# Kernel optimization log

Measured on AMD Instinct MI355X. Metric: run time of the kernel, lower is better.

Reference implementation:

```python
import jax, jax.numpy as jnp
import numpy as np

N = 200000
E = 3200000
DIN = 275
H = 64
A = 14


def setup_inputs() -> dict:
    key = jax.random.key(0)
    ks = jax.random.split(key, 16)
    s = 0.05
    return {
        "inputs": jax.random.normal(ks[0], (N, DIN), jnp.float32),
        "hidden_state": jax.random.normal(ks[1], (N, H), jnp.float32),
        "edge_index": jax.random.randint(ks[2], (2, E), 0, N, jnp.int64),
        # Encoder
        "enc_w": jax.random.normal(ks[3], (H, DIN), jnp.float32) * s,
        "enc_b": jnp.zeros((H,), jnp.float32),
        # GRUCell (torch layout: [3H, in], gate order r,z,n)
        "w_ih": jax.random.normal(ks[4], (3 * H, H), jnp.float32) * s,
        "w_hh": jax.random.normal(ks[5], (3 * H, H), jnp.float32) * s,
        "b_ih": jnp.zeros((3 * H,), jnp.float32),
        "b_hh": jnp.zeros((3 * H,), jnp.float32),
        # GCNConv layers (PyG: weight [out,in], bias added after aggregation)
        "g1_w": jax.random.normal(ks[6], (H, H), jnp.float32) * s,
        "g1_b": jnp.zeros((H,), jnp.float32),
        "g2_w": jax.random.normal(ks[7], (H, H), jnp.float32) * s,
        "g2_b": jnp.zeros((H,), jnp.float32),
        # Q head
        "q_w": jax.random.normal(ks[8], (A, H), jnp.float32) * s,
        "q_b": jnp.zeros((A,), jnp.float32),
    }


def _gru_cell(x, h, w_ih, w_hh, b_ih, b_hh):
    gi = x @ w_ih.T + b_ih  # [N, 3H]
    gh = h @ w_hh.T + b_hh
    i_r, i_z, i_n = jnp.split(gi, 3, axis=-1)
    h_r, h_z, h_n = jnp.split(gh, 3, axis=-1)
    r = jax.nn.sigmoid(i_r + h_r)
    z = jax.nn.sigmoid(i_z + h_z)
    n = jnp.tanh(i_n + r * h_n)
    return (1.0 - z) * n + z * h


def _gcn_conv(x, src, dst, norm, w, b, n_nodes):
    x = x @ w.T  # [N, H]
    msg = x[src] * norm[:, None]  # gather + normalize, [E', H]
    out = jax.ops.segment_sum(msg, dst, num_segments=n_nodes)
    return out + b


def reference(inputs, hidden_state, edge_index, enc_w, enc_b, w_ih, w_hh,
              b_ih, b_hh, g1_w, g1_b, g2_w, g2_b, q_w, q_b):
    n_nodes = inputs.shape[0]
    # Encoder
    h1 = jax.nn.relu(inputs @ enc_w.T + enc_b)
    # GRU
    h_in = hidden_state.reshape(-1, h1.shape[-1])
    h2 = _gru_cell(h1, h_in, w_ih, w_hh, b_ih, b_hh)
    # GCN: add self loops, symmetric normalization (PyG GCNConv defaults)
    loops = jnp.arange(n_nodes, dtype=edge_index.dtype)
    src = jnp.concatenate([edge_index[0], loops])
    dst = jnp.concatenate([edge_index[1], loops])
    deg = jax.ops.segment_sum(jnp.ones_like(dst, jnp.float32), dst,
                              num_segments=n_nodes)
    dis = jnp.where(deg > 0, jax.lax.rsqrt(jnp.maximum(deg, 1e-12)), 0.0)
    norm = dis[src] * dis[dst]
    x = _gcn_conv(h2, src, dst, norm, g1_w, g1_b, n_nodes)
    x = jax.nn.relu(x)  # dropout is identity in eval mode
    h3 = _gcn_conv(x, src, dst, norm, g2_w, g2_b, n_nodes)
    # Q head
    q = h3 @ q_w.T + q_b
    return q, h2
```

## Files before the change

### kernel.cpp

```cpp
#include <hip/hip_runtime.h>
#include <stdint.h>

#define H 64
#define DIN 275
#define AHEAD 14

typedef __attribute__((ext_vector_type(8))) short s16x8;
typedef __attribute__((ext_vector_type(4))) float f32x4;

#define MFMA16(a, b, c) __builtin_amdgcn_mfma_f32_16x16x32_bf16((a), (b), (c), 0, 0, 0)

__device__ __forceinline__ unsigned short bf16_rn(float x) {
  unsigned u = __float_as_uint(x);
  return (unsigned short)((u + 0x7FFFu + ((u >> 16) & 1u)) >> 16);
}
__device__ __forceinline__ float bf16f(unsigned short h) {
  return __uint_as_float(((unsigned)h) << 16);
}
__device__ __forceinline__ void cvt8(const float (&v)[8], s16x8& hi, s16x8& lo) {
#pragma unroll
  for (int j = 0; j < 8; ++j) {
    unsigned short h = bf16_rn(v[j]);
    hi[j] = (short)h;
    lo[j] = (short)bf16_rn(v[j] - bf16f(h));
  }
}

__global__ void k_packw(const float* __restrict__ W, int F_real, int K_real,
                        int KT, int FT, unsigned short* __restrict__ pack) {
  int idx = blockIdx.x * 256 + threadIdx.x;
  int total = KT * FT * 64;
  if (idx >= total) return;
  int lane = idx & 63;
  int t = idx >> 6;
  int ft = t % FT, kt = t / FT;
  int f = ft * 16 + (lane & 15);
  int kb = kt * 32 + (lane >> 4) * 8;
  unsigned short* base = pack + (size_t)(kt * FT + ft) * 2 * 512;
#pragma unroll
  for (int j = 0; j < 8; ++j) {
    int k = kb + j;
    float v = (f < F_real && k < K_real) ? W[(size_t)f * K_real + k] : 0.f;
    unsigned short h = bf16_rn(v);
    base[lane * 8 + j] = h;
    base[512 + lane * 8 + j] = bf16_rn(v - bf16f(h));
  }
}

__global__ void k_init_deg(int* __restrict__ deg, int n) {
  int i = blockIdx.x * 256 + threadIdx.x;
  if (i < n) deg[i] = 1;
}

__global__ void k_deg(const int* __restrict__ dst, int* __restrict__ deg, int e) {
  int i = blockIdx.x * 256 + threadIdx.x;
  if (i < e) atomicAdd(&deg[dst[i]], 1);
}

__global__ void k_scan1(const int* __restrict__ in, int* __restrict__ part,
                        int* __restrict__ bsums, int n) {
  int tid = threadIdx.x;
  int gid = blockIdx.x * 256 + tid;
  int v = (gid < n) ? in[gid] : 0;
  int lane = tid & 63, wv = tid >> 6;
  int x = v;
#pragma unroll
  for (int d = 1; d < 64; d <<= 1) {
    int y = __shfl_up(x, d, 64);
    if (lane >= d) x += y;
  }
  __shared__ int ws_[4];
  if (lane == 63) ws_[wv] = x;
  __syncthreads();
  int off = 0;
  for (int i = 0; i < wv; ++i) off += ws_[i];
  int incl = x + off;
  if (gid < n) part[gid] = incl - v;
  if (tid == 255) bsums[blockIdx.x] = incl;
}

__global__ void k_scan2(int* __restrict__ bsums, int nb) {
  int tid = threadIdx.x;
  int v = (tid < nb) ? bsums[tid] : 0;
  int lane = tid & 63, wv = tid >> 6;
  int x = v;
#pragma unroll
  for (int d = 1; d < 64; d <<= 1) {
    int y = __shfl_up(x, d, 64);
    if (lane >= d) x += y;
  }
  __shared__ int ws_[16];
  if (lane == 63) ws_[wv] = x;
  __syncthreads();
  int off = 0;
  for (int i = 0; i < wv; ++i) off += ws_[i];
  int incl = x + off;
  if (tid < nb) bsums[tid] = incl - v;
}

__global__ void k_scanfin(const int* __restrict__ part, const int* __restrict__ bsums,
                          const int* __restrict__ deg, int* __restrict__ row_start,
                          int* __restrict__ cursor, float* __restrict__ dis,
                          int n, int total) {
  int gid = blockIdx.x * 256 + threadIdx.x;
  if (gid < n) {
    int rs = part[gid] + bsums[gid >> 8];
    row_start[gid] = rs;
    cursor[gid] = rs;
    dis[gid] = rsqrtf((float)deg[gid]);
  } else if (gid == n) {
    row_start[n] = total;
  }
}

__global__ void k_fill(const int* __restrict__ src, const int* __restrict__ dst,
                       int* __restrict__ cursor, int* __restrict__ csr, int e, int n) {
  int i = blockIdx.x * 256 + threadIdx.x;
  if (i >= e + n) return;
  int s, d;
  if (i < e) { s = src[i]; d = dst[i]; }
  else       { s = i - e; d = s; }
  int pos = atomicAdd(&cursor[d], 1);
  csr[pos] = s;
}

__global__ __launch_bounds__(128, 2) void k_enc_mfma(
    const float* __restrict__ inp, const unsigned short* __restrict__ wp,
    const float* __restrict__ benc, float* __restrict__ h1o, int n) {
  __shared__ float lds[2][16 * DIN];
  int tid = threadIdx.x;
  int wv = tid >> 6, lane = tid & 63;
  long long node0 = ((long long)blockIdx.x * 2 + wv) * 16;
  if (node0 >= n) return;
  float* L = lds[wv];

  const float4* src = (const float4*)(inp + (size_t)node0 * DIN);
#pragma unroll
  for (int i = 0; i < 17; ++i) {
    float4 t = src[i * 64 + lane];
    *(float4*)(L + (i * 64 + lane) * 4) = t;
  }
  if (lane < 48) L[4352 + lane] = inp[(size_t)node0 * DIN + 4352 + lane];

  int r = lane & 15, kq = lane >> 4;
  f32x4 acc[4];
#pragma unroll
  for (int i = 0; i < 4; ++i) acc[i] = (f32x4){0.f, 0.f, 0.f, 0.f};

  const s16x8* bp = (const s16x8*)wp;
#pragma unroll
  for (int kc = 0; kc < 9; ++kc) {
    int kb = kc * 32 + kq * 8;
    float vv[8];
#pragma unroll
    for (int j = 0; j < 8; ++j) {
      int k = kb + j;
      float t = 0.f;
      if (kc < 8 || k < DIN) t = L[r * DIN + k];
      vv[j] = t;
    }
    s16x8 ah, al;
    cvt8(vv, ah, al);
#pragma unroll
    for (int ft = 0; ft < 4; ++ft) {
      s16x8 bh = bp[((kc * 4 + ft) * 2 + 0) * 64 + lane];
      s16x8 bl = bp[((kc * 4 + ft) * 2 + 1) * 64 + lane];
      acc[ft] = MFMA16(ah, bh, acc[ft]);
      acc[ft] = MFMA16(al, bh, acc[ft]);
      acc[ft] = MFMA16(ah, bl, acc[ft]);
    }
  }

  int fc = lane & 15, rq = lane >> 4;
#pragma unroll
  for (int ft = 0; ft < 4; ++ft) {
    float b = benc[ft * 16 + fc];
#pragma unroll
    for (int rg = 0; rg < 4; ++rg) {
      long long node = node0 + rq * 4 + rg;
      if (node < n)
        h1o[(size_t)node * 64 + ft * 16 + fc] = fmaxf(acc[ft][rg] + b, 0.f);
    }
  }
}

__global__ __launch_bounds__(256, 2) void k_gru_mfma(
    const float* __restrict__ h1g, const float* __restrict__ hid,
    const unsigned short* __restrict__ wpih, const unsigned short* __restrict__ wphh,
    const float* __restrict__ bih, const float* __restrict__ bhh,
    float* __restrict__ h2o, int n) {
  int tid = threadIdx.x;
  int wv = tid >> 6, lane = tid & 63;
  long long node0 = ((long long)blockIdx.x * 4 + wv) * 16;
  if (node0 >= n) return;
  int r = lane & 15, kq = lane >> 4;

  s16x8 xh[2], xl[2], hh[2], hl[2];
#pragma unroll
  for (int kc = 0; kc < 2; ++kc) {
    float vv[8];
    const float4* p = (const float4*)(h1g + (size_t)(node0 + r) * 64 + kc * 32 + kq * 8);
    float4 a = p[0], b = p[1];
    vv[0] = a.x; vv[1] = a.y; vv[2] = a.z; vv[3] = a.w;
    vv[4] = b.x; vv[5] = b.y; vv[6] = b.z; vv[7] = b.w;
    cvt8(vv, xh[kc], xl[kc]);
    const float4* q = (const float4*)(hid + (size_t)(node0 + r) * 64 + kc * 32 + kq * 8);
    float4 c = q[0], d = q[1];
    vv[0] = c.x; vv[1] = c.y; vv[2] = c.z; vv[3] = c.w;
    vv[4] = d.x; vv[5] = d.y; vv[6] = d.z; vv[7] = d.w;
    cvt8(vv, hh[kc], hl[kc]);
  }

  f32x4 ai[12], ag[12];
#pragma unroll
  for (int i = 0; i < 12; ++i) {
    ai[i] = (f32x4){0.f, 0.f, 0.f, 0.f};
    ag[i] = (f32x4){0.f, 0.f, 0.f, 0.f};
  }

  const s16x8* bpI = (const s16x8*)wpih;
  const s16x8* bpH = (const s16x8*)wphh;
#pragma unroll
  for (int kc = 0; kc < 2; ++kc) {
#pragma unroll
    for (int ft = 0; ft < 12; ++ft) {
      int t = (kc * 12 + ft) * 2;
      s16x8 bh = bpI[(t + 0) * 64 + lane];
      s16x8 bl = bpI[(t + 1) * 64 + lane];
      ai[ft] = MFMA16(xh[kc], bh, ai[ft]);
      ai[ft] = MFMA16(xl[kc], bh, ai[ft]);
      ai[ft] = MFMA16(xh[kc], bl, ai[ft]);
      s16x8 ch = bpH[(t + 0) * 64 + lane];
      s16x8 cl = bpH[(t + 1) * 64 + lane];
      ag[ft] = MFMA16(hh[kc], ch, ag[ft]);
      ag[ft] = MFMA16(hl[kc], ch, ag[ft]);
      ag[ft] = MFMA16(hh[kc], cl, ag[ft]);
    }
  }

  int fc = lane & 15, rq = lane >> 4;
#pragma unroll
  for (int ft = 0; ft < 4; ++ft) {
    int f = ft * 16 + fc;
    float bir = bih[f], biz = bih[64 + f], bin = bih[128 + f];
    float bhr = bhh[f], bhz = bhh[64 + f], bhn = bhh[128 + f];
#pragma unroll
    for (int rg = 0; rg < 4; ++rg) {
      long long node = node0 + rq * 4 + rg;
      float ir = ai[ft][rg] + bir, hr2 = ag[ft][rg] + bhr;
      float iz = ai[ft + 4][rg] + biz, hz = ag[ft + 4][rg] + bhz;
      float in2 = ai[ft + 8][rg] + bin, hn = ag[ft + 8][rg] + bhn;
      float rr = 1.f / (1.f + __expf(-(ir + hr2)));
      float zz = 1.f / (1.f + __expf(-(iz + hz)));
      float nn = tanhf(in2 + rr * hn);
      float hprev = hid[(size_t)node * 64 + f];
      if (node < n)
        h2o[(size_t)node * 64 + f] = (1.f - zz) * nn + zz * hprev;
    }
  }
}

__global__ __launch_bounds__(256, 4) void k_lin_mfma(
    const float* __restrict__ x, const unsigned short* __restrict__ wp,
    float* __restrict__ y, int n) {
  int tid = threadIdx.x;
  int wv = tid >> 6, lane = tid & 63;
  long long node0 = ((long long)blockIdx.x * 4 + wv) * 16;
  if (node0 >= n) return;
  int r = lane & 15, kq = lane >> 4;

  s16x8 ah[2], al[2];
#pragma unroll
  for (int kc = 0; kc < 2; ++kc) {
    float vv[8];
    const float4* p = (const float4*)(x + (size_t)(node0 + r) * 64 + kc * 32 + kq * 8);
    float4 a = p[0], b = p[1];
    vv[0] = a.x; vv[1] = a.y; vv[2] = a.z; vv[3] = a.w;
    vv[4] = b.x; vv[5] = b.y; vv[6] = b.z; vv[7] = b.w;
    cvt8(vv, ah[kc], al[kc]);
  }

  f32x4 acc[4];
#pragma unroll
  for (int i = 0; i < 4; ++i) acc[i] = (f32x4){0.f, 0.f, 0.f, 0.f};
  const s16x8* bp = (const s16x8*)wp;
#pragma unroll
  for (int kc = 0; kc < 2; ++kc) {
#pragma unroll
    for (int ft = 0; ft < 4; ++ft) {
      int t = (kc * 4 + ft) * 2;
      s16x8 bh = bp[(t + 0) * 64 + lane];
      s16x8 bl = bp[(t + 1) * 64 + lane];
      acc[ft] = MFMA16(ah[kc], bh, acc[ft]);
      acc[ft] = MFMA16(al[kc], bh, acc[ft]);
      acc[ft] = MFMA16(ah[kc], bl, acc[ft]);
    }
  }

  int fc = lane & 15, rq = lane >> 4;
#pragma unroll
  for (int ft = 0; ft < 4; ++ft)
#pragma unroll
    for (int rg = 0; rg < 4; ++rg) {
      long long node = node0 + rq * 4 + rg;
      if (node < n) y[(size_t)node * 64 + ft * 16 + fc] = acc[ft][rg];
    }
}

__global__ __launch_bounds__(256, 4) void k_q_mfma(
    const float* __restrict__ x, const unsigned short* __restrict__ wp,
    const float* __restrict__ qb, float* __restrict__ qout, int n) {
  int tid = threadIdx.x;
  int wv = tid >> 6, lane = tid & 63;
  long long node0 = ((long long)blockIdx.x * 4 + wv) * 16;
  if (node0 >= n) return;
  int r = lane & 15, kq = lane >> 4;

  s16x8 ah[2], al[2];
#pragma unroll
  for (int kc = 0; kc < 2; ++kc) {
    float vv[8];
    const float4* p = (const float4*)(x + (size_t)(node0 + r) * 64 + kc * 32 + kq * 8);
    float4 a = p[0], b = p[1];
    vv[0] = a.x; vv[1] = a.y; vv[2] = a.z; vv[3] = a.w;
    vv[4] = b.x; vv[5] = b.y; vv[6] = b.z; vv[7] = b.w;
    cvt8(vv, ah[kc], al[kc]);
  }

  f32x4 acc = (f32x4){0.f, 0.f, 0.f, 0.f};
  const s16x8* bp = (const s16x8*)wp;
#pragma unroll
  for (int kc = 0; kc < 2; ++kc) {
    s16x8 bh = bp[(kc * 2 + 0) * 64 + lane];
    s16x8 bl = bp[(kc * 2 + 1) * 64 + lane];
    acc = MFMA16(ah[kc], bh, acc);
    acc = MFMA16(al[kc], bh, acc);
    acc = MFMA16(ah[kc], bl, acc);
  }

  int fc = lane & 15, rq = lane >> 4;
  float b = (fc < AHEAD) ? qb[fc] : 0.f;
#pragma unroll
  for (int rg = 0; rg < 4; ++rg) {
    long long node = node0 + rq * 4 + rg;
    if (fc < AHEAD && node < n) qout[(size_t)node * AHEAD + fc] = acc[rg] + b;
  }
}

__global__ __launch_bounds__(256, 8) void k_agg(
    const float* __restrict__ y, const int* __restrict__ row_start,
    const int* __restrict__ csr, const float* __restrict__ dis,
    const float* __restrict__ bias, float* __restrict__ out,
    int n, int dorelu) {
  int t = blockIdx.x * 256 + threadIdx.x;
  int w = t >> 6;
  int lane = t & 63;
  if (w >= n) return;
  w = __builtin_amdgcn_readfirstlane(w);
  int beg = row_start[w], end = row_start[w + 1];
  float acc = 0.f;
  int i = beg;
  for (; i + 8 <= end; i += 8) {
    int s0 = csr[i + 0], s1 = csr[i + 1], s2 = csr[i + 2], s3 = csr[i + 3];
    int s4 = csr[i + 4], s5 = csr[i + 5], s6 = csr[i + 6], s7 = csr[i + 7];
    float n0 = dis[s0], n1 = dis[s1], n2 = dis[s2], n3 = dis[s3];
    float n4 = dis[s4], n5 = dis[s5], n6 = dis[s6], n7 = dis[s7];
    float v0 = y[(size_t)s0 * 64 + lane];
    float v1 = y[(size_t)s1 * 64 + lane];
    float v2 = y[(size_t)s2 * 64 + lane];
    float v3 = y[(size_t)s3 * 64 + lane];
    float v4 = y[(size_t)s4 * 64 + lane];
    float v5 = y[(size_t)s5 * 64 + lane];
    float v6 = y[(size_t)s6 * 64 + lane];
    float v7 = y[(size_t)s7 * 64 + lane];
    acc += v0 * n0 + v1 * n1 + v2 * n2 + v3 * n3;
    acc += v4 * n4 + v5 * n5 + v6 * n6 + v7 * n7;
  }
  for (; i + 4 <= end; i += 4) {
    int s0 = csr[i], s1 = csr[i + 1], s2 = csr[i + 2], s3 = csr[i + 3];
    float n0 = dis[s0], n1 = dis[s1], n2 = dis[s2], n3 = dis[s3];
    float v0 = y[(size_t)s0 * 64 + lane];
    float v1 = y[(size_t)s1 * 64 + lane];
    float v2 = y[(size_t)s2 * 64 + lane];
    float v3 = y[(size_t)s3 * 64 + lane];
    acc += v0 * n0 + v1 * n1 + v2 * n2 + v3 * n3;
  }
  for (; i < end; ++i) {
    int s = csr[i];
    acc += y[(size_t)s * 64 + lane] * dis[s];
  }
  acc = acc * dis[w] + bias[lane];
  if (dorelu) acc = fmaxf(acc, 0.f);
  out[(size_t)w * 64 + lane] = acc;
}

extern "C" void kernel_launch(void* const* d_in, const int* in_sizes, int n_in,
                              void* d_out, int out_size, void* d_ws, size_t ws_size,
                              hipStream_t stream) {
  const float* inp  = (const float*)d_in[0];
  const float* hid  = (const float*)d_in[1];
  const int*   eidx = (const int*)d_in[2];
  const float* encw = (const float*)d_in[3];
  const float* encb = (const float*)d_in[4];
  const float* wih  = (const float*)d_in[5];
  const float* whh  = (const float*)d_in[6];
  const float* bih  = (const float*)d_in[7];
  const float* bhh  = (const float*)d_in[8];
  const float* g1w  = (const float*)d_in[9];
  const float* g1b  = (const float*)d_in[10];
  const float* g2w  = (const float*)d_in[11];
  const float* g2b  = (const float*)d_in[12];
  const float* qw   = (const float*)d_in[13];
  const float* qb   = (const float*)d_in[14];

  int n = in_sizes[1] / H;
  int e = in_sizes[2] / 2;
  const int* esrc = eidx;
  const int* edst = eidx + e;

  float* qout = (float*)d_out;
  float* h2o  = (float*)d_out + (size_t)n * AHEAD;

  char* w = (char*)d_ws;
  unsigned short* p_enc = (unsigned short*)w; w += 9 * 4 * 2048;
  unsigned short* p_wih = (unsigned short*)w; w += 2 * 12 * 2048;
  unsigned short* p_whh = (unsigned short*)w; w += 2 * 12 * 2048;
  unsigned short* p_g1  = (unsigned short*)w; w += 2 * 4 * 2048;
  unsigned short* p_g2  = (unsigned short*)w; w += 2 * 4 * 2048;
  unsigned short* p_q   = (unsigned short*)w; w += 2 * 1 * 2048;
  int* deg       = (int*)w;   w += (size_t)n * 4;
  int* part      = (int*)w;   w += (size_t)n * 4;
  int* bsums     = (int*)w;   w += 4096;
  int* row_start = (int*)w;   w += ((size_t)n + 1) * 4;
  int* cursor    = (int*)w;   w += (size_t)n * 4;
  float* dis     = (float*)w; w += (size_t)n * 4;
  int* csr       = (int*)w;   w += (size_t)(e + n) * 4;
  w = (char*)(((uintptr_t)w + 15) & ~(uintptr_t)15);
  float* h1buf   = (float*)w; w += (size_t)n * H * 4;
  float* ybuf    = (float*)w; w += (size_t)n * H * 4;
  float* xbuf    = (float*)w; w += (size_t)n * H * 4;

  int nb = (n + 255) / 256;
  int total = e + n;

  hipLaunchKernelGGL(k_packw, dim3(9), dim3(256), 0, stream, encw, 64, DIN, 9, 4, p_enc);
  hipLaunchKernelGGL(k_packw, dim3(6), dim3(256), 0, stream, wih, 192, 64, 2, 12, p_wih);
  hipLaunchKernelGGL(k_packw, dim3(6), dim3(256), 0, stream, whh, 192, 64, 2, 12, p_whh);
  hipLaunchKernelGGL(k_packw, dim3(2), dim3(256), 0, stream, g1w, 64, 64, 2, 4, p_g1);
  hipLaunchKernelGGL(k_packw, dim3(2), dim3(256), 0, stream, g2w, 64, 64, 2, 4, p_g2);
  hipLaunchKernelGGL(k_packw, dim3(1), dim3(256), 0, stream, qw, AHEAD, 64, 2, 1, p_q);

  hipLaunchKernelGGL(k_init_deg, dim3(nb), dim3(256), 0, stream, deg, n);
  hipLaunchKernelGGL(k_deg, dim3((e + 255) / 256), dim3(256), 0, stream, edst, deg, e);
  hipLaunchKernelGGL(k_scan1, dim3(nb), dim3(256), 0, stream, deg, part, bsums, n);
  hipLaunchKernelGGL(k_scan2, dim3(1), dim3(1024), 0, stream, bsums, nb);
  hipLaunchKernelGGL(k_scanfin, dim3((n + 1 + 255) / 256), dim3(256), 0, stream,
                     part, bsums, deg, row_start, cursor, dis, n, total);
  hipLaunchKernelGGL(k_fill, dim3((total + 255) / 256), dim3(256), 0, stream,
                     esrc, edst, cursor, csr, e, n);

  hipLaunchKernelGGL(k_enc_mfma, dim3((n + 31) / 32), dim3(128), 0, stream,
                     inp, p_enc, encb, h1buf, n);
  hipLaunchKernelGGL(k_gru_mfma, dim3((n + 63) / 64), dim3(256), 0, stream,
                     h1buf, hid, p_wih, p_whh, bih, bhh, h2o, n);

  int aggblocks = (int)(((size_t)n * 64 + 255) / 256);
  hipLaunchKernelGGL(k_lin_mfma, dim3((n + 63) / 64), dim3(256), 0, stream, h2o, p_g1, ybuf, n);
  hipLaunchKernelGGL(k_agg, dim3(aggblocks), dim3(256), 0, stream,
                     ybuf, row_start, csr, dis, g1b, xbuf, n, 1);
  hipLaunchKernelGGL(k_lin_mfma, dim3((n + 63) / 64), dim3(256), 0, stream, xbuf, p_g2, ybuf, n);
  hipLaunchKernelGGL(k_agg, dim3(aggblocks), dim3(256), 0, stream,
                     ybuf, row_start, csr, dis, g2b, xbuf, n, 0);
  hipLaunchKernelGGL(k_q_mfma, dim3((n + 63) / 64), dim3(256), 0, stream, xbuf, p_q, qb, qout, n);
}
```

Baseline: 1.382 ms.

## Bucket edges by destination block before degree count and CSR fill

Replaces the global atomic degree count and random-order CSR fill with a two-level bucketing pass. Edges are histogrammed into 256-node buckets, scattered into per-bucket (src,dst) pairs, and degrees are then counted in shared memory per bucket. The CSR fill reads these locality-sorted pairs, so its atomics and writes hit nearby addresses. This adds extra passes and an 8-byte-per-edge pairs buffer. xbuf now aliases h1buf to save workspace.

```diff
diff --git a/kernel.cpp b/kernel.cpp
--- a/kernel.cpp
+++ b/kernel.cpp
@@ -4,6 +4,7 @@
 #define H 64
 #define DIN 275
 #define AHEAD 14
+#define EPB 8192
 
 typedef __attribute__((ext_vector_type(8))) short s16x8;
 typedef __attribute__((ext_vector_type(4))) float f32x4;
@@ -47,14 +48,91 @@
   }
 }
 
-__global__ void k_init_deg(int* __restrict__ deg, int n) {
+__global__ void k_zero(int* __restrict__ p) {
   int i = blockIdx.x * 256 + threadIdx.x;
-  if (i < n) deg[i] = 1;
-}
-
-__global__ void k_deg(const int* __restrict__ dst, int* __restrict__ deg, int e) {
-  int i = blockIdx.x * 256 + threadIdx.x;
-  if (i < e) atomicAdd(&deg[dst[i]], 1);
+  if (i < 1024) p[i] = 0;
+}
+
+__global__ void k_hist(const int* __restrict__ dst, int* __restrict__ bcnt, int e) {
+  __shared__ int h[1024];
+  for (int i = threadIdx.x; i < 1024; i += 256) h[i] = 0;
+  __syncthreads();
+  int stride = gridDim.x * 256;
+  for (int i = blockIdx.x * 256 + threadIdx.x; i < e; i += stride)
+    atomicAdd(&h[dst[i] >> 8], 1);
+  __syncthreads();
+  for (int i = threadIdx.x; i < 1024; i += 256)
+    if (h[i]) atomicAdd(&bcnt[i], h[i]);
+}
+
+__global__ void k_bscan(const int* __restrict__ cnt, int* __restrict__ base,
+                        int* __restrict__ cursor, int nb) {
+  int tid = threadIdx.x;
+  int v = (tid < nb) ? cnt[tid] : 0;
+  int lane = tid & 63, wv = tid >> 6;
+  int x = v;
+#pragma unroll
+  for (int d = 1; d < 64; d <<= 1) {
+    int y = __shfl_up(x, d, 64);
+    if (lane >= d) x += y;
+  }
+  __shared__ int ws_[16];
+  if (lane == 63) ws_[wv] = x;
+  __syncthreads();
+  int off = 0;
+  for (int i = 0; i < wv; ++i) off += ws_[i];
+  int excl = x + off - v;
+  if (tid < nb) { base[tid] = excl; cursor[tid] = excl; }
+}
+
+__global__ __launch_bounds__(256) void k_scatter(
+    const int* __restrict__ src, const int* __restrict__ dst,
+    int* __restrict__ cursor, int2* __restrict__ pairs, int e) {
+  __shared__ int hist[1024];
+  __shared__ int gbase[1024];
+  int tid = threadIdx.x;
+  int e0 = blockIdx.x * EPB;
+#pragma unroll
+  for (int q = 0; q < 4; ++q) hist[tid * 4 + q] = 0;
+  __syncthreads();
+  for (int k = 0; k < EPB / 256; ++k) {
+    int i = e0 + k * 256 + tid;
+    if (i < e) atomicAdd(&hist[dst[i] >> 8], 1);
+  }
+  __syncthreads();
+#pragma unroll
+  for (int q = 0; q < 4; ++q) {
+    int b = tid * 4 + q;
+    int c = hist[b];
+    if (c > 0) {
+      gbase[b] = atomicAdd(&cursor[b], c);
+      hist[b] = 0;
+    }
+  }
+  __syncthreads();
+  for (int k = 0; k < EPB / 256; ++k) {
+    int i = e0 + k * 256 + tid;
+    if (i < e) {
+      int s = src[i], d = dst[i];
+      int b = d >> 8;
+      int lr = atomicAdd(&hist[b], 1);
+      pairs[(size_t)gbase[b] + lr] = make_int2(s, d);
+    }
+  }
+}
+
+__global__ void k_degb(const int2* __restrict__ pairs, const int* __restrict__ bbase,
+                       const int* __restrict__ bcnt, int* __restrict__ deg, int n) {
+  __shared__ int c[256];
+  int b = blockIdx.x, tid = threadIdx.x;
+  c[tid] = 0;
+  __syncthreads();
+  int base = bbase[b], cnt = bcnt[b];
+  for (int i = tid; i < cnt; i += 256)
+    atomicAdd(&c[pairs[base + i].y & 255], 1);
+  __syncthreads();
+  int node = b * 256 + tid;
+  if (node < n) deg[node] = c[tid] + 1;
 }
 
 __global__ void k_scan1(const int* __restrict__ in, int* __restrict__ part,
@@ -113,12 +191,12 @@
   }
 }
 
-__global__ void k_fill(const int* __restrict__ src, const int* __restrict__ dst,
-                       int* __restrict__ cursor, int* __restrict__ csr, int e, int n) {
+__global__ void k_fill2(const int2* __restrict__ pairs, int* __restrict__ cursor,
+                        int* __restrict__ csr, int e, int n) {
   int i = blockIdx.x * 256 + threadIdx.x;
   if (i >= e + n) return;
   int s, d;
-  if (i < e) { s = src[i]; d = dst[i]; }
+  if (i < e) { int2 p = pairs[i]; s = p.x; d = p.y; }
   else       { s = i - e; d = s; }
   int pos = atomicAdd(&cursor[d], 1);
   csr[pos] = s;
@@ -421,6 +499,10 @@
   float* qout = (float*)d_out;
   float* h2o  = (float*)d_out + (size_t)n * AHEAD;
 
+  int nbuck = (n + 255) >> 8;
+  int nb = (n + 255) / 256;
+  int total = e + n;
+
   char* w = (char*)d_ws;
   unsigned short* p_enc = (unsigned short*)w; w += 9 * 4 * 2048;
   unsigned short* p_wih = (unsigned short*)w; w += 2 * 12 * 2048;
@@ -428,6 +510,9 @@
   unsigned short* p_g1  = (unsigned short*)w; w += 2 * 4 * 2048;
   unsigned short* p_g2  = (unsigned short*)w; w += 2 * 4 * 2048;
   unsigned short* p_q   = (unsigned short*)w; w += 2 * 1 * 2048;
+  int* bcnt      = (int*)w;   w += 4096 * 4;
+  int* bbase     = (int*)w;   w += 4096 * 4;
+  int* bcur      = (int*)w;   w += 4096 * 4;
   int* deg       = (int*)w;   w += (size_t)n * 4;
   int* part      = (int*)w;   w += (size_t)n * 4;
   int* bsums     = (int*)w;   w += 4096;
@@ -436,12 +521,10 @@
   float* dis     = (float*)w; w += (size_t)n * 4;
   int* csr       = (int*)w;   w += (size_t)(e + n) * 4;
   w = (char*)(((uintptr_t)w + 15) & ~(uintptr_t)15);
+  int2* pairs    = (int2*)w;  w += (size_t)e * 8;
   float* h1buf   = (float*)w; w += (size_t)n * H * 4;
   float* ybuf    = (float*)w; w += (size_t)n * H * 4;
-  float* xbuf    = (float*)w; w += (size_t)n * H * 4;
-
-  int nb = (n + 255) / 256;
-  int total = e + n;
+  float* xbuf    = h1buf;
 
   hipLaunchKernelGGL(k_packw, dim3(9), dim3(256), 0, stream, encw, 64, DIN, 9, 4, p_enc);
   hipLaunchKernelGGL(k_packw, dim3(6), dim3(256), 0, stream, wih, 192, 64, 2, 12, p_wih);
@@ -450,14 +533,18 @@
   hipLaunchKernelGGL(k_packw, dim3(2), dim3(256), 0, stream, g2w, 64, 64, 2, 4, p_g2);
   hipLaunchKernelGGL(k_packw, dim3(1), dim3(256), 0, stream, qw, AHEAD, 64, 2, 1, p_q);
 
-  hipLaunchKernelGGL(k_init_deg, dim3(nb), dim3(256), 0, stream, deg, n);
-  hipLaunchKernelGGL(k_deg, dim3((e + 255) / 256), dim3(256), 0, stream, edst, deg, e);
+  hipLaunchKernelGGL(k_zero, dim3(4), dim3(256), 0, stream, bcnt);
+  hipLaunchKernelGGL(k_hist, dim3(512), dim3(256), 0, stream, edst, bcnt, e);
+  hipLaunchKernelGGL(k_bscan, dim3(1), dim3(1024), 0, stream, bcnt, bbase, bcur, nbuck);
+  hipLaunchKernelGGL(k_scatter, dim3((e + EPB - 1) / EPB), dim3(256), 0, stream,
+                     esrc, edst, bcur, pairs, e);
+  hipLaunchKernelGGL(k_degb, dim3(nbuck), dim3(256), 0, stream, pairs, bbase, bcnt, deg, n);
   hipLaunchKernelGGL(k_scan1, dim3(nb), dim3(256), 0, stream, deg, part, bsums, n);
   hipLaunchKernelGGL(k_scan2, dim3(1), dim3(1024), 0, stream, bsums, nb);
   hipLaunchKernelGGL(k_scanfin, dim3((n + 1 + 255) / 256), dim3(256), 0, stream,
                      part, bsums, deg, row_start, cursor, dis, n, total);
-  hipLaunchKernelGGL(k_fill, dim3((total + 255) / 256), dim3(256), 0, stream,
-                     esrc, edst, cursor, csr, e, n);
+  hipLaunchKernelGGL(k_fill2, dim3((total + 255) / 256), dim3(256), 0, stream,
+                     pairs, cursor, csr, e, n);
 
   hipLaunchKernelGGL(k_enc_mfma, dim3((n + 31) / 32), dim3(128), 0, stream,
                      inp, p_enc, encb, h1buf, n);
```

Result: faster. 1.202 ms (-13.0%).
